# Kernel optimization log

Measured on AMD Instinct MI355X. Metric: run time of the kernel, lower is better.

## Reference

```python
import jax, jax.numpy as jnp
import numpy as np

D, R, C = 4, 6, 32
P = 2 * R + 1          # 13 (both pixel patch and memory patch, since memory_patch_R == R)
N = P * P              # 169
DIL_INT = 15


def corr_sampler(f1, f2, p, dil):
    """SpatialCorrelationSampler(kernel_size=1, patch_size=p, dilation_patch=dil).
    out[b,i,j,y,x] = sum_c f1[b,c,y,x] * f2[b,c, y+(i-Rp)*dil, x+(j-Rp)*dil] (zero pad)."""
    Rp = (p - 1) // 2
    pad = Rp * dil
    b, c, h, w = f1.shape
    f2p = jnp.pad(f2, ((0, 0), (0, 0), (pad, pad), (pad, pad)))
    outs = [jnp.einsum('bchw,bchw->bhw', f1, f2p[:, :, i * dil:i * dil + h, j * dil:j * dil + w])
            for i in range(p) for j in range(p)]
    return jnp.stack(outs, 1).reshape(b, p, p, h, w)


def bilinear_gather(im, ys, xs):
    """Bilinear sample im [b,c,H,W] at float coords ys,xs [b,N,h,w]; zeros outside."""
    H, W = im.shape[2], im.shape[3]
    y0 = jnp.floor(ys)
    x0 = jnp.floor(xs)
    wy = ys - y0
    wx = xs - x0

    def g(yi, xi):
        valid = ((yi >= 0) & (yi < H) & (xi >= 0) & (xi < W)).astype(im.dtype)
        yc = jnp.clip(yi, 0, H - 1).astype(jnp.int32)
        xc = jnp.clip(xi, 0, W - 1).astype(jnp.int32)
        out = jax.vmap(lambda imb, yb, xb: imb[:, yb, xb])(im, yc, xc)  # [b,c,N,h,w]
        return out * valid[:, None]

    return (g(y0, x0) * ((1 - wy) * (1 - wx))[:, None]
            + g(y0, x0 + 1) * ((1 - wy) * wx)[:, None]
            + g(y0 + 1, x0) * (wy * (1 - wx))[:, None]
            + g(y0 + 1, x0 + 1) * (wy * wx)[:, None])


def deform_im2col(im, offset, p):
    """Deformable im2col: for each output pixel (y,x) and kernel pos (ky,kx),
    bilinearly sample im at (y+ky-Rp+off_y, x+kx-Rp+off_x). offset [...,0]=x, [...,1]=y.
    Returns [b,c,p*p,h,w]."""
    b, c, h, w = im.shape
    Rp = (p - 1) // 2
    ky, kx = jnp.meshgrid(jnp.arange(p) - Rp, jnp.arange(p) - Rp, indexing='ij')
    ky = ky.reshape(-1).astype(im.dtype)
    kx = kx.reshape(-1).astype(im.dtype)
    ys = (jnp.arange(h, dtype=im.dtype)[None, None, :, None]
          + ky[None, :, None, None] + offset[..., 1][:, None])  # [b,N,h,w]
    xs = (jnp.arange(w, dtype=im.dtype)[None, None, None, :]
          + kx[None, :, None, None] + offset[..., 0][:, None])
    return bilinear_gather(im, ys, xs)


def unfold_patches(x, p, pad):
    """F.unfold(kernel_size=p, padding=pad) -> [b,c,p*p,h,w]."""
    b, c, h, w = x.shape
    xp = jnp.pad(x, ((0, 0), (0, 0), (pad, pad), (pad, pad)))
    cols = [xp[:, :, i:i + h, j:j + w] for i in range(p) for j in range(p)]
    return jnp.stack(cols, 2)


def _forward(feats_r, feats_t, quantized_r, ref_index, current_ind):
    ri = np.asarray(ref_index)
    ci = int(current_ind)
    diffs = [ci - int(x) for x in ri]
    nsearch = sum(1 for d in diffs if d > DIL_INT)
    dirates = [min(4, d // DIL_INT + 1) for d in diffs if d > DIL_INT]
    nref = feats_r.shape[0]
    b, c, h, w = feats_t.shape

    # offset grid: _y,_x = meshgrid(ij) so grid[...,0]=x-offset, grid[...,1]=y-offset
    _y, _x = jnp.meshgrid(jnp.arange(-R, R + 1), jnp.arange(-R, R + 1), indexing='ij')
    grid = jnp.stack([_x, _y], -1).astype(feats_t.dtype)  # [P,P,2]

    corrs_pixel = []
    offset0 = []
    for s in range(nsearch):
        cc = corr_sampler(feats_t, feats_r[s], P, dirates[s])             # [b,P,P,h,w]
        soft = jax.nn.softmax(cc.reshape(b, N, h * w), axis=1).reshape(b, P, P, h, w)
        off = jnp.einsum('bijhw,ijd->bhwd', soft, grid) * dirates[s]      # [b,h,w,2]
        offset0.append(off)
        col0 = deform_im2col(feats_r[s], off, P)                          # [b,c,N,h,w]
        corrs_pixel.append(jnp.einsum('bchw,bcnhw->bnhw', feats_t, col0).reshape(b, N, h * w))
    for ind in range(nsearch, nref):
        corrs_pixel.append(corr_sampler(feats_t, feats_r[ind], P, 1).reshape(b, N, h * w))

    corr_pixel = jax.nn.softmax(jnp.concatenate(corrs_pixel, 1), axis=1)  # [b,nref*N,h*w]

    # prep: float + stride-D subsampling (C-channel input, so no one-hot branch)
    qr = [quantized_r[i][:, :, ::D, ::D] for i in range(nref)]            # [b,C,h,w]
    cols = [deform_im2col(qr[i], offset0[i], P).reshape(b, C, N, h * w) for i in range(nsearch)]
    cols += [unfold_patches(qr[i], P, R).reshape(b, C, N, h * w) for i in range(nsearch, nref)]
    image_uf = jnp.concatenate(cols, 2)                                   # [b,C,nref*N,h*w]

    out = jnp.einsum('bkl,bckl->bcl', corr_pixel, image_uf).reshape(b, C, h, w)
    return out


def setup_inputs() -> dict:
    key = jax.random.key(0)
    k1, k2, k3 = jax.random.split(key, 3)
    feats_r = jax.random.normal(k1, (3, 1, 64, 56, 56), jnp.float32) * 0.2
    feats_t = jax.random.normal(k2, (1, 64, 56, 56), jnp.float32) * 0.2
    quantized_r = jax.random.uniform(k3, (3, 1, 32, 224, 224), jnp.float32)
    return {
        'feats_r': feats_r,
        'feats_t': feats_t,
        'quantized_r': quantized_r,
        'ref_index': np.array([0, 30, 39], dtype=np.int64),
        'current_ind': 40,
    }


def reference(feats_r, feats_t, quantized_r, ref_index, current_ind):
    return _forward(feats_r, feats_t, quantized_r, ref_index, current_ind)
```

## Files before the change

kernel.cpp:

```cpp
#include <hip/hip_runtime.h>

#define HW    56
#define NPIX  3136
#define CH    64
#define CQ    32
#define PS    13
#define NPOS  169
#define GS    14
#define NG    196
#define G1    15
#define NG1   225

typedef __attribute__((ext_vector_type(8))) short short8;
typedef __attribute__((ext_vector_type(8))) ushort ushort8;
typedef __attribute__((ext_vector_type(4))) float f32x4;

__device__ inline ushort f2bf(float f) {
  unsigned u = __float_as_uint(f);
  return (ushort)((u + 0x7fffu + ((u >> 16) & 1u)) >> 16);
}
__device__ inline float bf2f(ushort u) {
  return __uint_as_float((unsigned)u << 16);
}
__device__ inline void wave_sync() {
  asm volatile("s_waitcnt lgkmcnt(0)" ::: "memory");
  __builtin_amdgcn_sched_barrier(0);
}

__global__ __launch_bounds__(256) void prep_all(
    const float* __restrict__ ft_in,
    const float* __restrict__ fr_in,
    const float* __restrict__ q_in,
    ushort* __restrict__ ft_out,
    ushort* __restrict__ fr_out,
    ushort* __restrict__ qout,
    float* __restrict__ zrow) {
  __shared__ float smem[CQ * (HW + 1)];
  int bid = blockIdx.x, tid = threadIdx.x;
  if (bid < 784) {
    if (bid == 0 && tid < 64) zrow[tid] = 0.f;
    int m = bid / 196, t = bid - m * 196;
    int row0 = (t / 98) * 32;
    int col0 = (t - (t / 98) * 98) * 32;
    const float* src = (m == 0) ? ft_in : fr_in + (size_t)(m - 1) * CH * NPIX;
    ushort* dst      = (m == 0) ? ft_out : fr_out + (size_t)(m - 1) * NPIX * CH;
    int ty = tid >> 3, tx4 = (tid & 7) * 4;
    f32x4 v = *(const f32x4*)&src[(size_t)(row0 + ty) * NPIX + col0 + tx4];
    *(f32x4*)&smem[ty * 33 + tx4] = v;
    __syncthreads();
    int px = tid >> 3, c4 = (tid & 7) * 4;
    ushort4 o;
    o.x = f2bf(smem[(c4 + 0) * 33 + px]);
    o.y = f2bf(smem[(c4 + 1) * 33 + px]);
    o.z = f2bf(smem[(c4 + 2) * 33 + px]);
    o.w = f2bf(smem[(c4 + 3) * 33 + px]);
    *(ushort4*)&dst[(size_t)(col0 + px) * CH + row0 + c4] = o;
  } else {
    int q = bid - 784;
    int r = q / HW, yy = q - r * HW;
    for (int idx = tid; idx < CQ * HW; idx += 256) {
      int c = idx / HW, xx = idx - c * HW;
      smem[c * (HW + 1) + xx] = q_in[((size_t)(r * CQ + c) * 224 + yy * 4) * 224 + xx * 4];
    }
    __syncthreads();
    for (int idx = tid; idx < CQ * HW; idx += 256) {
      int xx = idx >> 5, c = idx & 31;
      qout[(size_t)r * NPIX * CQ + (size_t)(yy * HW + xx) * CQ + c] = f2bf(smem[c * (HW + 1) + xx]);
    }
  }
}

__global__ __launch_bounds__(256, 4) void colorizer_main(
    const ushort* __restrict__ ftb,
    const ushort* __restrict__ frb,
    const ushort* __restrict__ qrb,
    const ushort* __restrict__ zrow,
    float* __restrict__ out)
{
  __shared__ float C1[1024];
  __shared__ float C2[1024];
  __shared__ float W1[1024];
  __shared__ float W2[1024];
  __shared__ int   pw[4 * 832];
  __shared__ float Sas[4];
  __shared__ float fqr0[128];
  __shared__ float red2[1024];

  int tid = threadIdx.x;
  int wid = tid >> 6, lane = tid & 63;
  int mrow = lane & 15, klane = lane >> 4;

  int b = blockIdx.x;
  int swz = (b & 7) * 98 + (b >> 3);
  int bx = swz % 28, by = swz / 28;
  int Y0 = by * 2, X0 = bx * 2;
  int dy = wid >> 1, dx = wid & 1;
  int y = Y0 + dy, x = X0 + dx;
  int pix = y * HW + x;

  int*   wb   = pw + wid * 832;
  float* e    = (float*)wb;
  float* D    = (float*)(wb + 176);
  float* wg   = (float*)(wb + 384);
  int*   offg = wb + 608;
  float* cc   = (float*)offg;

  if (lane < 16) offg[208 + lane] = -1;
#pragma unroll
  for (int k = 0; k < 4; ++k) { W1[tid + 256 * k] = 0.f; W2[tid + 256 * k] = 0.f; }

  const ushort* frb0 = frb;
  const ushort* frb1 = frb + (size_t)NPIX * CH;
  const ushort* frb2 = frb + (size_t)2 * NPIX * CH;
  const ushort* qr0b = qrb;
  const ushort* qr1b = qrb + (size_t)NPIX * CQ;
  const ushort* qr2b = qrb + (size_t)2 * NPIX * CQ;

  const ushort* fb = ftb + (size_t)pix * CH;
  const ushort* plo = (mrow == 0) ? (fb + klane * 8) : zrow;
  const ushort* phi = (mrow == 0) ? (fb + 32 + klane * 8) : zrow;
  short8 b_lo = *(const short8*)plo;
  short8 b_hi = *(const short8*)phi;

  const ushort* fb4 = (mrow < 4)
      ? (ftb + (size_t)((Y0 + (mrow >> 1)) * HW + X0 + (mrow & 1)) * CH)
      : zrow;
  short8 b4_lo = *(const short8*)(fb4 + klane * 8);
  short8 b4_hi = *(const short8*)(fb4 + 32 + klane * 8);

#pragma unroll
  for (int k = 0; k < 8; ++k) {
    int j = wid + 4 * k;
    if (j < 30) {
      int r = (j >= 15);
      int t = j - r * 15;
      int g = t * 16 + mrow;
      int gy = g / G1, gx = g - gy * G1;
      int sy = Y0 - 6 + gy, sx = X0 - 6 + gx;
      bool v = (g < NG1) && ((unsigned)sy < HW) && ((unsigned)sx < HW);
      const ushort* base = r ? frb2 : frb1;
      const ushort* rb = v ? (base + (size_t)(sy * HW + sx) * CH) : zrow;
      short8 alo = *(const short8*)(rb + klane * 8);
      short8 ahi = *(const short8*)(rb + 32 + klane * 8);
      f32x4 acc = {0.f, 0.f, 0.f, 0.f};
      acc = __builtin_amdgcn_mfma_f32_16x16x32_bf16(alo, b4_lo, acc, 0, 0, 0);
      acc = __builtin_amdgcn_mfma_f32_16x16x32_bf16(ahi, b4_hi, acc, 0, 0, 0);
      int col = lane & 15;
      if (col < 4) {
        float* Cd = r ? C2 : C1;
        int row0 = t * 16 + (lane >> 4) * 4;
#pragma unroll
        for (int q = 0; q < 4; ++q) Cd[(row0 + q) * 4 + col] = acc[q];
      }
    }
  }
  __syncthreads();

#pragma unroll
  for (int g = 0; g < 11; ++g) {
    int d = g * 16 + mrow;
    int ii = d / PS, jj = d - ii * PS;
    int sy = y + (ii - 6) * 3, sx = x + (jj - 6) * 3;
    bool v = (d < NPOS) && ((unsigned)sy < HW) && ((unsigned)sx < HW);
    const ushort* rb = v ? (frb0 + (size_t)(sy * HW + sx) * CH) : zrow;
    short8 alo = *(const short8*)(rb + klane * 8);
    short8 ahi = *(const short8*)(rb + 32 + klane * 8);
    f32x4 acc = {0.f, 0.f, 0.f, 0.f};
    acc = __builtin_amdgcn_mfma_f32_16x16x32_bf16(alo, b_lo, acc, 0, 0, 0);
    acc = __builtin_amdgcn_mfma_f32_16x16x32_bf16(ahi, b_hi, acc, 0, 0, 0);
    if (mrow == 0) *(f32x4*)&cc[g * 16 + klane * 4] = acc;
  }
  wave_sync();

  float vs[3];
  float mx = -1e30f;
#pragma unroll
  for (int k = 0; k < 3; ++k) {
    int id = lane + 64 * k;
    float c = (id < NPOS) ? cc[id] : -1e30f;
    vs[k] = c;
    mx = fmaxf(mx, c);
  }
#pragma unroll
  for (int o = 1; o < 64; o <<= 1) mx = fmaxf(mx, __shfl_xor(mx, o));
  float se = 0.f, sxe = 0.f, sye = 0.f;
#pragma unroll
  for (int k = 0; k < 3; ++k) {
    int id = lane + 64 * k;
    if (id < NPOS) {
      float ex = __expf(vs[k] - mx);
      int pi = id / PS, pj = id - pi * PS;
      se += ex;
      sxe += ex * (float)(pj - 6);
      sye += ex * (float)(pi - 6);
    }
  }
#pragma unroll
  for (int o = 1; o < 64; o <<= 1) {
    se  += __shfl_xor(se, o);
    sxe += __shfl_xor(sxe, o);
    sye += __shfl_xor(sye, o);
  }
  float offx = 3.f * sxe / se;
  float offy = 3.f * sye / se;

  float fy0 = floorf(offy), fx0 = floorf(offx);
  int   iy0 = (int)fy0,     ix0 = (int)fx0;
  float wyf = offy - fy0,   wxf = offx - fx0;
  float w00 = (1.f - wyf) * (1.f - wxf), w01 = (1.f - wyf) * wxf;
  float w10 = wyf * (1.f - wxf),         w11 = wyf * wxf;

#pragma unroll
  for (int g = 0; g < 13; ++g) {
    int d = g * 16 + mrow;
    int a = d / GS, bq = d - a * GS;
    int sy = y + iy0 + a - 6, sx = x + ix0 + bq - 6;
    bool vA = (d < NG) && ((unsigned)sy < HW) && ((unsigned)sx < HW);
    int roA = sy * HW + sx;
    const ushort* rbA = vA ? (frb0 + (size_t)roA * CH) : zrow;
    short8 aAlo = *(const short8*)(rbA + klane * 8);
    short8 aAhi = *(const short8*)(rbA + 32 + klane * 8);
    f32x4 accA = {0.f, 0.f, 0.f, 0.f};
    accA = __builtin_amdgcn_mfma_f32_16x16x32_bf16(aAlo, b_lo, accA, 0, 0, 0);
    accA = __builtin_amdgcn_mfma_f32_16x16x32_bf16(aAhi, b_hi, accA, 0, 0, 0);
    if (klane == 0) offg[d] = vA ? roA : -1;
    if (mrow == 0) *(f32x4*)&D[g * 16 + klane * 4] = accA;
  }
  wave_sync();

#pragma unroll
  for (int k = 0; k < 3; ++k) {
    int id = lane + 64 * k;
    if (id < NPOS) {
      int pi = id / PS, pj = id - (id / PS) * PS;
      e[id] = w00 * D[pi * GS + pj]       + w01 * D[pi * GS + pj + 1]
            + w10 * D[(pi + 1) * GS + pj] + w11 * D[(pi + 1) * GS + pj + 1];
    } else if (id < 176) {
      e[id] = -1e30f;
    }
  }
  wave_sync();

  float mx2 = -1e30f;
#pragma unroll
  for (int k = 0; k < 3; ++k) {
    int id = lane + 64 * k;
    if (id < 176) mx2 = fmaxf(mx2, e[id]);
    if (id < NPOS) {
      int ii = id / PS, jj = id - (id / PS) * PS;
      int g = (ii + dy) * G1 + (jj + dx);
      mx2 = fmaxf(mx2, fmaxf(C1[g * 4 + wid], C2[g * 4 + wid]));
    }
  }
#pragma unroll
  for (int o = 1; o < 64; o <<= 1) mx2 = fmaxf(mx2, __shfl_xor(mx2, o));
  float ps = 0.f;
#pragma unroll
  for (int k = 0; k < 3; ++k) {
    int id = lane + 64 * k;
    if (id < 176) {
      float ex = __expf(e[id] - mx2);
      e[id] = ex;
      ps += ex;
    }
    if (id < NPOS) {
      int ii = id / PS, jj = id - (id / PS) * PS;
      int g = (ii + dy) * G1 + (jj + dx);
      float e1c = __expf(C1[g * 4 + wid] - mx2);
      float e2c = __expf(C2[g * 4 + wid] - mx2);
      W1[g * 4 + wid] = e1c;
      W2[g * 4 + wid] = e2c;
      ps += e1c + e2c;
    }
  }
#pragma unroll
  for (int o = 1; o < 64; o <<= 1) ps += __shfl_xor(ps, o);
  if (lane == 0) Sas[wid] = ps;
  wave_sync();

#pragma unroll
  for (int k = 0; k < 4; ++k) {
    int t = lane + 64 * k;
    if (t < 224) {
      float acc = 0.f;
      if (t < NG) {
        int a = t / GS, bq2 = t - (t / GS) * GS;
        if (a < PS && bq2 < PS) acc += w00 * e[a * PS + bq2];
        if (a < PS && bq2 >= 1) acc += w01 * e[a * PS + bq2 - 1];
        if (a >= 1 && bq2 < PS) acc += w10 * e[(a - 1) * PS + bq2];
        if (a >= 1 && bq2 >= 1) acc += w11 * e[(a - 1) * PS + bq2 - 1];
      }
      wg[t] = acc;
    }
  }
  wave_sync();

  int slot = lane >> 2, ln4 = lane & 3;
  float acc8[8];
#pragma unroll
  for (int c = 0; c < 8; ++c) acc8[c] = 0.f;
#pragma unroll
  for (int k = 0; k < 14; ++k) {
    int d = slot + k * 16;
    int ro = offg[d];
    if (ro >= 0) {
      float w = wg[d];
      ushort8 u = *(const ushort8*)(qr0b + (size_t)ro * CQ + ln4 * 8);
#pragma unroll
      for (int c = 0; c < 8; ++c) acc8[c] = fmaf(w, bf2f(u[c]), acc8[c]);
    }
  }
#pragma unroll
  for (int o = 4; o <= 32; o <<= 1)
#pragma unroll
    for (int c = 0; c < 8; ++c) acc8[c] += __shfl_xor(acc8[c], o);
  if (lane < 4) {
#pragma unroll
    for (int c = 0; c < 8; ++c) fqr0[wid * 32 + lane * 8 + c] = acc8[c];
  }
  __syncthreads();

  {
    int s = tid >> 3, ref = (tid >> 2) & 1, h = tid & 3;
    const ushort* qb = ref ? qr2b : qr1b;
    const float*  Wr = ref ? W2 : W1;
    float a12[4][8];
#pragma unroll
    for (int p = 0; p < 4; ++p)
#pragma unroll
      for (int c = 0; c < 8; ++c) a12[p][c] = 0.f;
#pragma unroll
    for (int i = 0; i < 8; ++i) {
      int g = s + 32 * i;
      if (g < NG1) {
        int gy = g / G1, gx = g - gy * G1;
        int sy = Y0 - 6 + gy, sx = X0 - 6 + gx;
        if (((unsigned)sy < HW) && ((unsigned)sx < HW)) {
          ushort8 u = *(const ushort8*)(qb + (size_t)(sy * HW + sx) * CQ + h * 8);
          f32x4 wv = *(const f32x4*)&Wr[g * 4];
          float qv[8];
#pragma unroll
          for (int c = 0; c < 8; ++c) qv[c] = bf2f(u[c]);
#pragma unroll
          for (int p = 0; p < 4; ++p)
#pragma unroll
            for (int c = 0; c < 8; ++c) a12[p][c] = fmaf(wv[p], qv[c], a12[p][c]);
        }
      }
    }
#pragma unroll
    for (int o = 8; o <= 32; o <<= 1)
#pragma unroll
      for (int p = 0; p < 4; ++p)
#pragma unroll
        for (int c = 0; c < 8; ++c) a12[p][c] += __shfl_xor(a12[p][c], o);
    if (lane < 8) {
      int rh = lane;
#pragma unroll
      for (int p = 0; p < 4; ++p)
#pragma unroll
        for (int c = 0; c < 8; ++c)
          red2[wid * 256 + rh * 32 + p * 8 + c] = a12[p][c];
    }
  }
  __syncthreads();

  if (tid < 128) {
    int p = tid >> 5, c = tid & 31;
    int h = c >> 3, c8 = c & 7;
    float tot = fqr0[p * 32 + c];
#pragma unroll
    for (int w = 0; w < 4; ++w)
      tot += red2[w * 256 + (0 * 4 + h) * 32 + p * 8 + c8]
           + red2[w * 256 + (1 * 4 + h) * 32 + p * 8 + c8];
    int pidx = (Y0 + (p >> 1)) * HW + X0 + (p & 1);
    out[(size_t)c * NPIX + pidx] = tot / Sas[p];
  }
}

extern "C" void kernel_launch(void* const* d_in, const int* in_sizes, int n_in,
                              void* d_out, int out_size, void* d_ws, size_t ws_size,
                              hipStream_t stream) {
  const float* feats_r     = (const float*)d_in[0];
  const float* feats_t     = (const float*)d_in[1];
  const float* quantized_r = (const float*)d_in[2];

  ushort* ftb = (ushort*)d_ws;
  ushort* frb = ftb + 200704;
  ushort* qrb = frb + 602112;
  float*  zro = (float*)(qrb + 301056);

  prep_all<<<952, 256, 0, stream>>>(feats_t, feats_r, quantized_r,
                                    ftb, frb, qrb, zro);
  colorizer_main<<<784, 256, 0, stream>>>(ftb, frb, qrb, (const ushort*)zro,
                                          (float*)d_out);
}
```

Measured before the change: 48.76 us.

## Split fused colorizer into correlation, offset, deform and accumulation kernels

Replaces the single fused colorizer kernel with four kernels. The first computes all correlation exponentials row-wise with MFMA from shared-memory tiles and stores them to a global buffer. Small kernels then derive the offsets and do the deformable sampling, and a final per-row kernel accumulates the two unfold references. It also drops the max-subtraction from the softmax, relying on small correlation magnitudes. In exchange it adds extra launches, a large intermediate E buffer written and re-read through global memory, and a very low-parallelism final kernel (56 blocks).

```diff
diff --git a/kernel.cpp b/kernel.cpp
--- a/kernel.cpp
+++ b/kernel.cpp
@@ -8,8 +8,6 @@
 #define NPOS  169
 #define GS    14
 #define NG    196
-#define G1    15
-#define NG1   225
 
 typedef __attribute__((ext_vector_type(8))) short short8;
 typedef __attribute__((ext_vector_type(8))) ushort ushort8;
@@ -70,51 +68,145 @@
   }
 }
 
-__global__ __launch_bounds__(256, 4) void colorizer_main(
+__global__ __launch_bounds__(256) void corr_exp(
+    const ushort* __restrict__ ftb,
+    const ushort* __restrict__ frb,
+    float* __restrict__ E) {
+  __shared__ ushort lA[64 * 72];
+  __shared__ ushort lB[112 * 72];
+  __shared__ float etl[4][208];
+
+  int bid = blockIdx.x;
+  int r = bid / 728;
+  int rem = bid - r * 728;
+  int y = rem / PS;
+  int dy = rem - y * PS;
+  int dil = (r == 0) ? 3 : 1;
+  int ys = y + (dy - 6) * dil;
+  bool ysv = ((unsigned)ys < HW);
+
+  int tid = threadIdx.x;
+  int wid = tid >> 6, lane = tid & 63;
+  const ushort* fr_r = frb + (size_t)r * NPIX * CH;
+
+#pragma unroll
+  for (int k = 0; k < 2; ++k) {
+    int idx = tid + 256 * k;
+    int xr = idx >> 3, ch = idx & 7;
+    if (xr < HW)
+      *(ushort8*)&lA[xr * 72 + ch * 8] =
+          *(const ushort8*)&ftb[((size_t)(y * HW + xr)) * CH + ch * 8];
+  }
+#pragma unroll
+  for (int k = 0; k < 4; ++k) {
+    int idx = tid + 256 * k;
+    if (idx < 112 * 8) {
+      int cB = idx >> 3, ch = idx & 7;
+      int xB = cB - 20;
+      ushort8 v = {0, 0, 0, 0, 0, 0, 0, 0};
+      if (ysv && (unsigned)xB < HW)
+        v = *(const ushort8*)&fr_r[((size_t)(ys * HW + xB)) * CH + ch * 8];
+      *(ushort8*)&lB[cB * 72 + ch * 8] = v;
+    }
+  }
+  __syncthreads();
+
+  int x0 = (wid < 3) ? wid * 16 : 40;
+  int mr = lane & 15, kl = lane >> 4;
+  short8 a_lo = *(const short8*)&lA[(x0 + mr) * 72 + kl * 8];
+  short8 a_hi = *(const short8*)&lA[(x0 + mr) * 72 + 32 + kl * 8];
+
+  int ntile = (dil == 1) ? 2 : 4;
+  int base = (dil == 1) ? -6 : -18;
+  for (int t = 0; t < ntile; ++t) {
+    int xB0 = x0 + base + 16 * t;
+    short8 b_lo = *(const short8*)&lB[(xB0 + mr + 20) * 72 + kl * 8];
+    short8 b_hi = *(const short8*)&lB[(xB0 + mr + 20) * 72 + 32 + kl * 8];
+    f32x4 acc = {0.f, 0.f, 0.f, 0.f};
+    acc = __builtin_amdgcn_mfma_f32_16x16x32_bf16(a_lo, b_lo, acc, 0, 0, 0);
+    acc = __builtin_amdgcn_mfma_f32_16x16x32_bf16(a_hi, b_hi, acc, 0, 0, 0);
+    int j = lane & 15;
+#pragma unroll
+    for (int q = 0; q < 4; ++q) {
+      int i = (lane >> 4) * 4 + q;
+      int delta = base + 16 * t + j - i;
+      if (dil == 1) {
+        if (delta >= -6 && delta <= 6) etl[wid][(delta + 6) * 16 + i] = __expf(acc[q]);
+      } else {
+        if (delta >= -18 && delta <= 18 && (delta % 3) == 0)
+          etl[wid][(delta / 3 + 6) * 16 + i] = __expf(acc[q]);
+      }
+    }
+  }
+  wave_sync();
+
+  size_t pbase = (size_t)(y * HW + x0);
+#pragma unroll
+  for (int k = 0; k < 4; ++k) {
+    int idx = lane + 64 * k;
+    if (idx < 208) {
+      int jj = idx >> 4, i = idx & 15;
+      E[((size_t)r * NPOS + dy * PS + jj) * NPIX + pbase + i] = etl[wid][jj * 16 + i];
+    }
+  }
+}
+
+__global__ __launch_bounds__(256) void offset_kernel(
+    const float* __restrict__ E, float* __restrict__ params) {
+  int p = blockIdx.x * 256 + threadIdx.x;
+  if (p >= NPIX) return;
+  float se = 0.f, sxe = 0.f, sye = 0.f;
+#pragma unroll 13
+  for (int d = 0; d < NPOS; ++d) {
+    float v = E[(size_t)d * NPIX + p];
+    int pi = d / PS, pj = d - pi * PS;
+    se += v;
+    sxe += v * (float)(pj - 6);
+    sye += v * (float)(pi - 6);
+  }
+  float offx = 3.f * sxe / se, offy = 3.f * sye / se;
+  float fy0 = floorf(offy), fx0 = floorf(offx);
+  float wy = offy - fy0, wx = offx - fx0;
+  float s12 = 0.f;
+#pragma unroll 13
+  for (int d = 0; d < 2 * NPOS; ++d)
+    s12 += E[(size_t)(NPOS + d) * NPIX + p];
+  params[p * 8 + 0] = fy0;
+  params[p * 8 + 1] = fx0;
+  params[p * 8 + 2] = (1.f - wy) * (1.f - wx);
+  params[p * 8 + 3] = (1.f - wy) * wx;
+  params[p * 8 + 4] = wy * (1.f - wx);
+  params[p * 8 + 5] = wy * wx;
+  params[p * 8 + 6] = s12;
+  params[p * 8 + 7] = 0.f;
+}
+
+__global__ __launch_bounds__(256, 4) void deform_kernel(
     const ushort* __restrict__ ftb,
     const ushort* __restrict__ frb,
     const ushort* __restrict__ qrb,
     const ushort* __restrict__ zrow,
-    float* __restrict__ out)
-{
-  __shared__ float C1[1024];
-  __shared__ float C2[1024];
-  __shared__ float W1[1024];
-  __shared__ float W2[1024];
-  __shared__ int   pw[4 * 832];
-  __shared__ float Sas[4];
-  __shared__ float fqr0[128];
-  __shared__ float red2[1024];
-
-  int tid = threadIdx.x;
-  int wid = tid >> 6, lane = tid & 63;
+    const float* __restrict__ params,
+    float* __restrict__ out0,
+    float* __restrict__ Stot) {
+  __shared__ int pwm[4 * 832];
+  int tid = threadIdx.x, wid = tid >> 6, lane = tid & 63;
+  int pix = blockIdx.x * 4 + wid;
+  int y = pix / HW, x = pix - y * HW;
   int mrow = lane & 15, klane = lane >> 4;
 
-  int b = blockIdx.x;
-  int swz = (b & 7) * 98 + (b >> 3);
-  int bx = swz % 28, by = swz / 28;
-  int Y0 = by * 2, X0 = bx * 2;
-  int dy = wid >> 1, dx = wid & 1;
-  int y = Y0 + dy, x = X0 + dx;
-  int pix = y * HW + x;
-
-  int*   wb   = pw + wid * 832;
-  float* e    = (float*)wb;
-  float* D    = (float*)(wb + 176);
-  float* wg   = (float*)(wb + 384);
-  int*   offg = wb + 608;
-  float* cc   = (float*)offg;
-
+  int* wb = pwm + wid * 832;
+  float* e  = (float*)wb;
+  float* D  = (float*)(wb + 176);
+  float* wg = (float*)(wb + 384);
+  int* offg = wb + 608;
   if (lane < 16) offg[208 + lane] = -1;
-#pragma unroll
-  for (int k = 0; k < 4; ++k) { W1[tid + 256 * k] = 0.f; W2[tid + 256 * k] = 0.f; }
-
-  const ushort* frb0 = frb;
-  const ushort* frb1 = frb + (size_t)NPIX * CH;
-  const ushort* frb2 = frb + (size_t)2 * NPIX * CH;
-  const ushort* qr0b = qrb;
-  const ushort* qr1b = qrb + (size_t)NPIX * CQ;
-  const ushort* qr2b = qrb + (size_t)2 * NPIX * CQ;
+
+  float fy0 = params[pix * 8 + 0], fx0 = params[pix * 8 + 1];
+  float w00 = params[pix * 8 + 2], w01 = params[pix * 8 + 3];
+  float w10 = params[pix * 8 + 4], w11 = params[pix * 8 + 5];
+  float s12 = params[pix * 8 + 6];
+  int iy0 = (int)fy0, ix0 = (int)fx0;
 
   const ushort* fb = ftb + (size_t)pix * CH;
   const ushort* plo = (mrow == 0) ? (fb + klane * 8) : zrow;
@@ -122,160 +214,39 @@
   short8 b_lo = *(const short8*)plo;
   short8 b_hi = *(const short8*)phi;
 
-  const ushort* fb4 = (mrow < 4)
-      ? (ftb + (size_t)((Y0 + (mrow >> 1)) * HW + X0 + (mrow & 1)) * CH)
-      : zrow;
-  short8 b4_lo = *(const short8*)(fb4 + klane * 8);
-  short8 b4_hi = *(const short8*)(fb4 + 32 + klane * 8);
-
-#pragma unroll
-  for (int k = 0; k < 8; ++k) {
-    int j = wid + 4 * k;
-    if (j < 30) {
-      int r = (j >= 15);
-      int t = j - r * 15;
-      int g = t * 16 + mrow;
-      int gy = g / G1, gx = g - gy * G1;
-      int sy = Y0 - 6 + gy, sx = X0 - 6 + gx;
-      bool v = (g < NG1) && ((unsigned)sy < HW) && ((unsigned)sx < HW);
-      const ushort* base = r ? frb2 : frb1;
-      const ushort* rb = v ? (base + (size_t)(sy * HW + sx) * CH) : zrow;
-      short8 alo = *(const short8*)(rb + klane * 8);
-      short8 ahi = *(const short8*)(rb + 32 + klane * 8);
-      f32x4 acc = {0.f, 0.f, 0.f, 0.f};
-      acc = __builtin_amdgcn_mfma_f32_16x16x32_bf16(alo, b4_lo, acc, 0, 0, 0);
-      acc = __builtin_amdgcn_mfma_f32_16x16x32_bf16(ahi, b4_hi, acc, 0, 0, 0);
-      int col = lane & 15;
-      if (col < 4) {
-        float* Cd = r ? C2 : C1;
-        int row0 = t * 16 + (lane >> 4) * 4;
-#pragma unroll
-        for (int q = 0; q < 4; ++q) Cd[(row0 + q) * 4 + col] = acc[q];
-      }
-    }
-  }
-  __syncthreads();
-
-#pragma unroll
-  for (int g = 0; g < 11; ++g) {
+#pragma unroll
+  for (int g = 0; g < 13; ++g) {
     int d = g * 16 + mrow;
-    int ii = d / PS, jj = d - ii * PS;
-    int sy = y + (ii - 6) * 3, sx = x + (jj - 6) * 3;
-    bool v = (d < NPOS) && ((unsigned)sy < HW) && ((unsigned)sx < HW);
-    const ushort* rb = v ? (frb0 + (size_t)(sy * HW + sx) * CH) : zrow;
+    int a = d / GS, bq = d - a * GS;
+    int sy = y + iy0 + a - 6, sx = x + ix0 + bq - 6;
+    bool v = (d < NG) && ((unsigned)sy < HW) && ((unsigned)sx < HW);
+    int ro = sy * HW + sx;
+    const ushort* rb = v ? (frb + (size_t)ro * CH) : zrow;
     short8 alo = *(const short8*)(rb + klane * 8);
     short8 ahi = *(const short8*)(rb + 32 + klane * 8);
     f32x4 acc = {0.f, 0.f, 0.f, 0.f};
     acc = __builtin_amdgcn_mfma_f32_16x16x32_bf16(alo, b_lo, acc, 0, 0, 0);
     acc = __builtin_amdgcn_mfma_f32_16x16x32_bf16(ahi, b_hi, acc, 0, 0, 0);
-    if (mrow == 0) *(f32x4*)&cc[g * 16 + klane * 4] = acc;
+    if (klane == 0) offg[d] = v ? ro : -1;
+    if (mrow == 0) *(f32x4*)&D[g * 16 + klane * 4] = acc;
   }
   wave_sync();
 
-  float vs[3];
-  float mx = -1e30f;
-#pragma unroll
-  for (int k = 0; k < 3; ++k) {
-    int id = lane + 64 * k;
-    float c = (id < NPOS) ? cc[id] : -1e30f;
-    vs[k] = c;
-    mx = fmaxf(mx, c);
-  }
-#pragma unroll
-  for (int o = 1; o < 64; o <<= 1) mx = fmaxf(mx, __shfl_xor(mx, o));
-  float se = 0.f, sxe = 0.f, sye = 0.f;
-#pragma unroll
-  for (int k = 0; k < 3; ++k) {
-    int id = lane + 64 * k;
-    if (id < NPOS) {
-      float ex = __expf(vs[k] - mx);
-      int pi = id / PS, pj = id - pi * PS;
-      se += ex;
-      sxe += ex * (float)(pj - 6);
-      sye += ex * (float)(pi - 6);
-    }
-  }
-#pragma unroll
-  for (int o = 1; o < 64; o <<= 1) {
-    se  += __shfl_xor(se, o);
-    sxe += __shfl_xor(sxe, o);
-    sye += __shfl_xor(sye, o);
-  }
-  float offx = 3.f * sxe / se;
-  float offy = 3.f * sye / se;
-
-  float fy0 = floorf(offy), fx0 = floorf(offx);
-  int   iy0 = (int)fy0,     ix0 = (int)fx0;
-  float wyf = offy - fy0,   wxf = offx - fx0;
-  float w00 = (1.f - wyf) * (1.f - wxf), w01 = (1.f - wyf) * wxf;
-  float w10 = wyf * (1.f - wxf),         w11 = wyf * wxf;
-
-#pragma unroll
-  for (int g = 0; g < 13; ++g) {
-    int d = g * 16 + mrow;
-    int a = d / GS, bq = d - a * GS;
-    int sy = y + iy0 + a - 6, sx = x + ix0 + bq - 6;
-    bool vA = (d < NG) && ((unsigned)sy < HW) && ((unsigned)sx < HW);
-    int roA = sy * HW + sx;
-    const ushort* rbA = vA ? (frb0 + (size_t)roA * CH) : zrow;
-    short8 aAlo = *(const short8*)(rbA + klane * 8);
-    short8 aAhi = *(const short8*)(rbA + 32 + klane * 8);
-    f32x4 accA = {0.f, 0.f, 0.f, 0.f};
-    accA = __builtin_amdgcn_mfma_f32_16x16x32_bf16(aAlo, b_lo, accA, 0, 0, 0);
-    accA = __builtin_amdgcn_mfma_f32_16x16x32_bf16(aAhi, b_hi, accA, 0, 0, 0);
-    if (klane == 0) offg[d] = vA ? roA : -1;
-    if (mrow == 0) *(f32x4*)&D[g * 16 + klane * 4] = accA;
-  }
-  wave_sync();
-
+  float ps = 0.f;
 #pragma unroll
   for (int k = 0; k < 3; ++k) {
     int id = lane + 64 * k;
     if (id < NPOS) {
       int pi = id / PS, pj = id - (id / PS) * PS;
-      e[id] = w00 * D[pi * GS + pj]       + w01 * D[pi * GS + pj + 1]
-            + w10 * D[(pi + 1) * GS + pj] + w11 * D[(pi + 1) * GS + pj + 1];
-    } else if (id < 176) {
-      e[id] = -1e30f;
-    }
-  }
-  wave_sync();
-
-  float mx2 = -1e30f;
-#pragma unroll
-  for (int k = 0; k < 3; ++k) {
-    int id = lane + 64 * k;
-    if (id < 176) mx2 = fmaxf(mx2, e[id]);
-    if (id < NPOS) {
-      int ii = id / PS, jj = id - (id / PS) * PS;
-      int g = (ii + dy) * G1 + (jj + dx);
-      mx2 = fmaxf(mx2, fmaxf(C1[g * 4 + wid], C2[g * 4 + wid]));
-    }
-  }
-#pragma unroll
-  for (int o = 1; o < 64; o <<= 1) mx2 = fmaxf(mx2, __shfl_xor(mx2, o));
-  float ps = 0.f;
-#pragma unroll
-  for (int k = 0; k < 3; ++k) {
-    int id = lane + 64 * k;
-    if (id < 176) {
-      float ex = __expf(e[id] - mx2);
+      float c0 = w00 * D[pi * GS + pj]       + w01 * D[pi * GS + pj + 1]
+               + w10 * D[(pi + 1) * GS + pj] + w11 * D[(pi + 1) * GS + pj + 1];
+      float ex = __expf(c0);
       e[id] = ex;
       ps += ex;
     }
-    if (id < NPOS) {
-      int ii = id / PS, jj = id - (id / PS) * PS;
-      int g = (ii + dy) * G1 + (jj + dx);
-      float e1c = __expf(C1[g * 4 + wid] - mx2);
-      float e2c = __expf(C2[g * 4 + wid] - mx2);
-      W1[g * 4 + wid] = e1c;
-      W2[g * 4 + wid] = e2c;
-      ps += e1c + e2c;
-    }
   }
 #pragma unroll
   for (int o = 1; o < 64; o <<= 1) ps += __shfl_xor(ps, o);
-  if (lane == 0) Sas[wid] = ps;
   wave_sync();
 
 #pragma unroll
@@ -284,11 +255,11 @@
     if (t < 224) {
       float acc = 0.f;
       if (t < NG) {
-        int a = t / GS, bq2 = t - (t / GS) * GS;
-        if (a < PS && bq2 < PS) acc += w00 * e[a * PS + bq2];
-        if (a < PS && bq2 >= 1) acc += w01 * e[a * PS + bq2 - 1];
-        if (a >= 1 && bq2 < PS) acc += w10 * e[(a - 1) * PS + bq2];
-        if (a >= 1 && bq2 >= 1) acc += w11 * e[(a - 1) * PS + bq2 - 1];
+        int a = t / GS, b2 = t - (t / GS) * GS;
+        if (a < PS && b2 < PS) acc += w00 * e[a * PS + b2];
+        if (a < PS && b2 >= 1) acc += w01 * e[a * PS + b2 - 1];
+        if (a >= 1 && b2 < PS) acc += w10 * e[(a - 1) * PS + b2];
+        if (a >= 1 && b2 >= 1) acc += w11 * e[(a - 1) * PS + b2 - 1];
       }
       wg[t] = acc;
     }
@@ -305,7 +276,7 @@
     int ro = offg[d];
     if (ro >= 0) {
       float w = wg[d];
-      ushort8 u = *(const ushort8*)(qr0b + (size_t)ro * CQ + ln4 * 8);
+      ushort8 u = *(const ushort8*)(qrb + (size_t)ro * CQ + ln4 * 8);
 #pragma unroll
       for (int c = 0; c < 8; ++c) acc8[c] = fmaf(w, bf2f(u[c]), acc8[c]);
     }
@@ -315,66 +286,64 @@
 #pragma unroll
     for (int c = 0; c < 8; ++c) acc8[c] += __shfl_xor(acc8[c], o);
   if (lane < 4) {
-#pragma unroll
-    for (int c = 0; c < 8; ++c) fqr0[wid * 32 + lane * 8 + c] = acc8[c];
-  }
-  __syncthreads();
-
-  {
-    int s = tid >> 3, ref = (tid >> 2) & 1, h = tid & 3;
-    const ushort* qb = ref ? qr2b : qr1b;
-    const float*  Wr = ref ? W2 : W1;
-    float a12[4][8];
-#pragma unroll
-    for (int p = 0; p < 4; ++p)
-#pragma unroll
-      for (int c = 0; c < 8; ++c) a12[p][c] = 0.f;
-#pragma unroll
-    for (int i = 0; i < 8; ++i) {
-      int g = s + 32 * i;
-      if (g < NG1) {
-        int gy = g / G1, gx = g - gy * G1;
-        int sy = Y0 - 6 + gy, sx = X0 - 6 + gx;
-        if (((unsigned)sy < HW) && ((unsigned)sx < HW)) {
-          ushort8 u = *(const ushort8*)(qb + (size_t)(sy * HW + sx) * CQ + h * 8);
-          f32x4 wv = *(const f32x4*)&Wr[g * 4];
-          float qv[8];
-#pragma unroll
-          for (int c = 0; c < 8; ++c) qv[c] = bf2f(u[c]);
-#pragma unroll
-          for (int p = 0; p < 4; ++p)
-#pragma unroll
-            for (int c = 0; c < 8; ++c) a12[p][c] = fmaf(wv[p], qv[c], a12[p][c]);
+    f32x4 lo = {acc8[0], acc8[1], acc8[2], acc8[3]};
+    f32x4 hi = {acc8[4], acc8[5], acc8[6], acc8[7]};
+    *(f32x4*)&out0[(size_t)pix * 32 + lane * 8]     = lo;
+    *(f32x4*)&out0[(size_t)pix * 32 + lane * 8 + 4] = hi;
+  }
+  if (lane == 0) Stot[pix] = ps + s12;
+}
+
+__global__ __launch_bounds__(256) void accum_final(
+    const float* __restrict__ E,
+    const ushort* __restrict__ qrb,
+    const float* __restrict__ out0,
+    const float* __restrict__ Stot,
+    float* __restrict__ out) {
+  __shared__ float ew[PS * HW];
+  int yb = blockIdx.x;
+  int tid = threadIdx.x;
+  int xx = tid >> 2, c8 = tid & 3;
+  bool act = (xx < HW);
+  float acc8[8];
+#pragma unroll
+  for (int c = 0; c < 8; ++c) acc8[c] = 0.f;
+
+  for (int r = 1; r <= 2; ++r) {
+    const ushort* qb = qrb + (size_t)r * NPIX * CQ;
+    const float* Er = E + (size_t)r * NPOS * NPIX;
+    for (int dy = 0; dy < PS; ++dy) {
+      int ys = yb + dy - 6;
+      if ((unsigned)ys < HW) {
+        __syncthreads();
+        for (int idx = tid; idx < PS * HW; idx += 256) {
+          int dxs = idx / HW, xs = idx - dxs * HW;
+          ew[idx] = Er[(size_t)(dy * PS + dxs) * NPIX + yb * HW + xs];
+        }
+        __syncthreads();
+        if (act) {
+#pragma unroll
+          for (int dx = 0; dx < PS; ++dx) {
+            int xs = xx + dx - 6;
+            if ((unsigned)xs < HW) {
+              float w = ew[dx * HW + xx];
+              ushort8 u = *(const ushort8*)&qb[((size_t)(ys * HW + xs)) * CQ + c8 * 8];
+#pragma unroll
+              for (int c = 0; c < 8; ++c) acc8[c] = fmaf(w, bf2f(u[c]), acc8[c]);
+            }
+          }
         }
       }
     }
-#pragma unroll
-    for (int o = 8; o <= 32; o <<= 1)
-#pragma unroll
-      for (int p = 0; p < 4; ++p)
-#pragma unroll
-        for (int c = 0; c < 8; ++c) a12[p][c] += __shfl_xor(a12[p][c], o);
-    if (lane < 8) {
-      int rh = lane;
-#pragma unroll
-      for (int p = 0; p < 4; ++p)
-#pragma unroll
-        for (int c = 0; c < 8; ++c)
-          red2[wid * 256 + rh * 32 + p * 8 + c] = a12[p][c];
-    }
-  }
-  __syncthreads();
-
-  if (tid < 128) {
-    int p = tid >> 5, c = tid & 31;
-    int h = c >> 3, c8 = c & 7;
-    float tot = fqr0[p * 32 + c];
-#pragma unroll
-    for (int w = 0; w < 4; ++w)
-      tot += red2[w * 256 + (0 * 4 + h) * 32 + p * 8 + c8]
-           + red2[w * 256 + (1 * 4 + h) * 32 + p * 8 + c8];
-    int pidx = (Y0 + (p >> 1)) * HW + X0 + (p & 1);
-    out[(size_t)c * NPIX + pidx] = tot / Sas[p];
+  }
+  if (act) {
+    int pix = yb * HW + xx;
+    float inv = 1.f / Stot[pix];
+#pragma unroll
+    for (int c = 0; c < 8; ++c) {
+      float tot = acc8[c] + out0[(size_t)pix * 32 + c8 * 8 + c];
+      out[(size_t)(c8 * 8 + c) * NPIX + pix] = tot * inv;
+    }
   }
 }
 
@@ -388,10 +357,17 @@
   ushort* ftb = (ushort*)d_ws;
   ushort* frb = ftb + 200704;
   ushort* qrb = frb + 602112;
-  float*  zro = (float*)(qrb + 301056);
+  float* zro    = (float*)(qrb + 301056);
+  float* E      = zro + 64;
+  float* params = E + 1589952;
+  float* out0   = params + 25088;
+  float* Stot   = out0 + 100352;
 
   prep_all<<<952, 256, 0, stream>>>(feats_t, feats_r, quantized_r,
                                     ftb, frb, qrb, zro);
-  colorizer_main<<<784, 256, 0, stream>>>(ftb, frb, qrb, (const ushort*)zro,
-                                          (float*)d_out);
-}
+  corr_exp<<<2184, 256, 0, stream>>>(ftb, frb, E);
+  offset_kernel<<<13, 256, 0, stream>>>(E, params);
+  deform_kernel<<<784, 256, 0, stream>>>(ftb, frb, qrb, (const ushort*)zro,
+                                         params, out0, Stot);
+  accum_final<<<56, 256, 0, stream>>>(E, qrb, out0, Stot, (float*)d_out);
+}
```

Result: slower. 149.0 us (+205.6%).
